# Optimization experiments

Hardware: AMD Instinct MI355X
Metric: run time of the kernel (lower is better)

Reference implementation:

```python
import jax, jax.numpy as jnp
import numpy as np

D = 1352      # d_model
H = 8         # n_heads
HD = D // H   # 169 head dim
L = 7         # n_layers
E = 4         # experts per layer
DFF = 2704    # expert hidden (2*d_model)
NUM_OPS = 16
OP_START = 0
B, S = 1, 1024


def setup_inputs() -> dict:
    key = jax.random.key(0)
    ks = jax.random.split(key, 8)
    g = lambda k, shape, sc: (jax.random.normal(k, shape, jnp.float32) * sc)
    return {
        "x": g(ks[0], (B, S, D), 1.0),
        "ln1_g": jnp.ones((L, D), jnp.float32),
        "ln1_b": jnp.zeros((L, D), jnp.float32),
        "wqkv": g(ks[1], (L, D, 3 * D), 0.02),
        "bqkv": jnp.zeros((L, 3 * D), jnp.float32),
        "wo": g(ks[2], (L, D, D), 0.02),
        "bo": jnp.zeros((L, D), jnp.float32),
        "ln2_g": jnp.ones((L, D), jnp.float32),
        "ln2_b": jnp.zeros((L, D), jnp.float32),
        "w1": g(ks[3], (L, E, D, DFF), 0.02),
        "b1": jnp.zeros((L, E, DFF), jnp.float32),
        "w2": g(ks[4], (L, E, DFF, D), 0.02),
        "b2": jnp.zeros((L, E, D), jnp.float32),
    }


def _layer_norm(x, g, b, eps=1e-5):
    mu = jnp.mean(x, axis=-1, keepdims=True)
    var = jnp.mean(jnp.square(x - mu), axis=-1, keepdims=True)
    return (x - mu) * jax.lax.rsqrt(var + eps) * g + b


def reference(x, ln1_g, ln1_b, wqkv, bqkv, wo, bo, ln2_g, ln2_b, w1, b1, w2, b2):
    Bx, Sx, _ = x.shape
    # deterministic opcode routing: one-hot slab -> opcode id -> expert id
    op_ids = jnp.argmax(x[..., OP_START:OP_START + NUM_OPS], axis=-1)  # [B,S]
    mask = jax.nn.one_hot(op_ids % E, E, dtype=x.dtype)                # [B,S,E]
    causal = jnp.tril(jnp.ones((Sx, Sx), bool))
    neg = jnp.asarray(-1e9, x.dtype)
    scale = jnp.asarray(1.0 / np.sqrt(HD), x.dtype)

    def block(h, p):
        g1, bb1, wq, bq, w_o, b_o, g2, bb2, W1, B1, W2, B2 = p
        # --- causal multi-head attention (pre-LN, residual) ---
        a = _layer_norm(h, g1, bb1)
        qkv = a @ wq + bq                                   # [B,S,3D]
        q, k, v = jnp.split(qkv, 3, axis=-1)
        q = q.reshape(Bx, Sx, H, HD).transpose(0, 2, 1, 3)  # [B,H,S,HD]
        k = k.reshape(Bx, Sx, H, HD).transpose(0, 2, 1, 3)
        v = v.reshape(Bx, Sx, H, HD).transpose(0, 2, 1, 3)
        scores = jnp.einsum("bhqd,bhkd->bhqk", q, k) * scale
        scores = jnp.where(causal, scores, neg)
        attn = jax.nn.softmax(scores, axis=-1)
        o = jnp.einsum("bhqk,bhkd->bhqd", attn, v)
        o = o.transpose(0, 2, 1, 3).reshape(Bx, Sx, D) @ w_o + b_o
        h = h + o
        # --- opcode-routed MoE FFN (dense masked compute, one-hot dispatch) ---
        m = _layer_norm(h, g2, bb2)
        hid = jax.nn.relu(jnp.einsum("bsd,edf->bsef", m, W1) + B1)   # [B,S,E,DFF]
        y = jnp.einsum("bsef,efd->bsed", hid, W2) + B2               # [B,S,E,D]
        h = h + jnp.einsum("bsed,bse->bsd", y, mask)
        return h, None

    out, _ = jax.lax.scan(
        block, x,
        (ln1_g, ln1_b, wqkv, bqkv, wo, bo, ln2_g, ln2_b, w1, b1, w2, b2),
    )
    return out
```

## Files before the change

### kernel.cpp

```cpp
#include <hip/hip_runtime.h>
#include <hip/hip_bf16.h>
#include <cstdint>

#define S_LEN 1024
#define DMODEL 1352
#define TD 4056
#define DFFN 2704
#define NHEAD 8
#define HDIM 169
#define NLAYER 7
#define LDAP 1408
#define KP2 2752
#define QS 1536
#define HP 192

typedef __attribute__((ext_vector_type(8))) short short8;
typedef __attribute__((ext_vector_type(4))) float f32x4;
typedef __attribute__((ext_vector_type(2))) unsigned short us2;
typedef __attribute__((ext_vector_type(4))) unsigned short us4;

__device__ __forceinline__ unsigned short f2bf(float f) {
    union { float f; unsigned int u; } c; c.f = f;
    unsigned int r = (c.u + 0x7fffu + ((c.u >> 16) & 1u)) >> 16;
    return (unsigned short)r;
}

__device__ __forceinline__ float bf2f(unsigned short u) {
    union { unsigned int u; float f; } c; c.u = (unsigned int)u << 16;
    return c.f;
}

__device__ __forceinline__ void g2l16(const void* g, void* l) {
    __builtin_amdgcn_global_load_lds((__attribute__((address_space(1))) void*)g,
                                     (__attribute__((address_space(3))) void*)l,
                                     16, 0, 0);
}

__global__ __launch_bounds__(256) void route_k(const float* __restrict__ x,
                                               int* __restrict__ perm,
                                               int* __restrict__ pcnt) {
    const int tid = threadIdx.x;
    const int lane = tid & 63;
    const int w = tid >> 6;
    for (int i = tid; i < 4096; i += 256) perm[i] = -1;
    __syncthreads();
    int base = 0;
    for (int c = 0; c < 16; ++c) {
        const int t = c * 64 + lane;
        const float* xr = x + (long long)t * DMODEL;
        float best = xr[0]; int bi = 0;
        #pragma unroll
        for (int j = 1; j < 16; ++j) { float v = xr[j]; if (v > best) { best = v; bi = j; } }
        const bool match = ((bi & 3) == w);
        unsigned long long mb = __ballot(match);
        int pos = __popcll(mb & ((1ull << lane) - 1ull));
        if (match) perm[w * 1024 + base + pos] = t;
        base += __popcll(mb);
    }
    if (lane == 0) pcnt[w] = (base + 127) & ~127;
}

__device__ __forceinline__ void tconv_tile64(const float* __restrict__ src,
    unsigned short* __restrict__ dst, int K, int N, int Kp, int kt, int nt,
    float (*t)[65])
{
    const int k0 = kt * 32, n0 = nt * 64;
    const int lane = threadIdx.x & 63, wv = threadIdx.x >> 6;
    #pragma unroll
    for (int i = 0; i < 8; ++i) {
        const int k = k0 + wv * 8 + i;
        const int n = n0 + lane;
        t[wv * 8 + i][lane] = (k < K && n < N) ? src[(long long)k * N + n] : 0.f;
    }
    __syncthreads();
    #pragma unroll
    for (int p = 0; p < 4; ++p) {
        const int nr = p * 16 + (threadIdx.x >> 4);
        const int kp = (threadIdx.x & 15) * 2;
        const int n = n0 + nr;
        if (n < N) {
            us2 wv2; wv2.x = f2bf(t[kp][nr]); wv2.y = f2bf(t[kp + 1][nr]);
            *(us2*)&dst[(long long)n * Kp + k0 + kp] = wv2;
        }
    }
}

__device__ __forceinline__ void ln_row(const float* __restrict__ h,
    const float* __restrict__ g, const float* __restrict__ b,
    unsigned short* __restrict__ out, int row, float* sA, float* sB)
{
    const float* hr = h + (long long)row * DMODEL;
    float s = 0.f, s2 = 0.f;
    for (int j = threadIdx.x; j < DMODEL; j += 256) { float v = hr[j]; s += v; s2 += v * v; }
    #pragma unroll
    for (int o = 32; o; o >>= 1) { s += __shfl_xor(s, o, 64); s2 += __shfl_xor(s2, o, 64); }
    const int lane = threadIdx.x & 63, wid = threadIdx.x >> 6;
    if (lane == 0) { sA[wid] = s; sB[wid] = s2; }
    __syncthreads();
    s = sA[0] + sA[1] + sA[2] + sA[3];
    s2 = sB[0] + sB[1] + sB[2] + sB[3];
    const float mu = s / DMODEL;
    const float rstd = rsqrtf(fmaxf(s2 / DMODEL - mu * mu, 0.f) + 1e-5f);
    unsigned short* orow = out + (long long)row * LDAP;
    for (int j = threadIdx.x; j < LDAP; j += 256) {
        float v = (j < DMODEL) ? (hr[j] - mu) * rstd * g[j] + b[j] : 0.f;
        orow[j] = f2bf(v);
    }
}

#define NB1_QKV (44 * 64)
#define NB1_WO  (44 * 22)
#define NB2_W1  (44 * 43 * 4)
#define NB2_W2  (86 * 22 * 4)

__global__ __launch_bounds__(256) void prep1_k(
    const float* __restrict__ wqkv_l, const float* __restrict__ wo_l,
    unsigned short* __restrict__ wqkvT, unsigned short* __restrict__ woT,
    const float* __restrict__ h, const float* __restrict__ g,
    const float* __restrict__ bb, unsigned short* __restrict__ lnA)
{
    __shared__ __align__(16) float t[32][65];
    __shared__ float sA[4], sB[4];
    int b = blockIdx.x;
    if (b < NB1_QKV) {
        tconv_tile64(wqkv_l, wqkvT, DMODEL, TD, LDAP, b % 44, b / 44, t);
        return;
    }
    b -= NB1_QKV;
    if (b < NB1_WO) {
        tconv_tile64(wo_l, woT, DMODEL, DMODEL, LDAP, b % 44, b / 44, t);
        return;
    }
    b -= NB1_WO;
    ln_row(h, g, bb, lnA, b, sA, sB);
}

__global__ __launch_bounds__(256) void prep2_k(
    const float* __restrict__ w1_l, const float* __restrict__ w2_l,
    unsigned short* __restrict__ w1T, unsigned short* __restrict__ w2T,
    const float* __restrict__ h, const float* __restrict__ g,
    const float* __restrict__ bb, unsigned short* __restrict__ lnA)
{
    __shared__ __align__(16) float t[32][65];
    __shared__ float sA[4], sB[4];
    int b = blockIdx.x;
    if (b < NB2_W1) {
        const int kt = b % 44, rem = b / 44;
        const int nt = rem % 43, z = rem / 43;
        tconv_tile64(w1_l + (long long)z * DMODEL * DFFN,
                     w1T + (long long)z * 2816 * LDAP,
                     DMODEL, DFFN, LDAP, kt, nt, t);
        return;
    }
    b -= NB2_W1;
    if (b < NB2_W2) {
        const int kt = b % 86, rem = b / 86;
        const int nt = rem % 22, z = rem / 22;
        tconv_tile64(w2_l + (long long)z * DFFN * DMODEL,
                     w2T + (long long)z * 1408 * KP2,
                     DFFN, DMODEL, KP2, kt, nt, t);
        return;
    }
    b -= NB2_W2;
    ln_row(h, g, bb, lnA, b, sA, sB);
}

__global__ __launch_bounds__(256) void softmax_k(const unsigned short* __restrict__ scores,
                                                 unsigned short* __restrict__ P,
                                                 float scale) {
    const int i = blockIdx.x;
    const long long rb = ((long long)blockIdx.y * 1024 + i) * 1024;
    const unsigned short* srow = scores + rb;
    unsigned short* prow = P + rb;
    const int n = i + 1;
    const int j0 = threadIdx.x * 4;

    us4 raw = *(const us4*)&srow[j0];
    float v[4];
    #pragma unroll
    for (int e = 0; e < 4; ++e)
        v[e] = (j0 + e < n) ? bf2f(raw[e]) * scale : -1e30f;

    float mx = fmaxf(fmaxf(v[0], v[1]), fmaxf(v[2], v[3]));
    __shared__ float sA[4], sB[4];
    #pragma unroll
    for (int o = 32; o; o >>= 1) mx = fmaxf(mx, __shfl_xor(mx, o, 64));
    const int lane = threadIdx.x & 63, wid = threadIdx.x >> 6;
    if (lane == 0) sA[wid] = mx;
    __syncthreads();
    mx = fmaxf(fmaxf(sA[0], sA[1]), fmaxf(sA[2], sA[3]));

    float p[4]; float sum = 0.f;
    #pragma unroll
    for (int e = 0; e < 4; ++e) {
        p[e] = (j0 + e < n) ? __expf(v[e] - mx) : 0.f;
        sum += p[e];
    }
    #pragma unroll
    for (int o = 32; o; o >>= 1) sum += __shfl_xor(sum, o, 64);
    if (lane == 0) sB[wid] = sum;
    __syncthreads();
    const float inv = 1.f / (sB[0] + sB[1] + sB[2] + sB[3]);

    us4 out;
    #pragma unroll
    for (int e = 0; e < 4; ++e) out[e] = f2bf(p[e] * inv);
    *(us4*)&prow[j0] = out;
}

template<int EPI, bool GATHER, int CAUSAL>
__global__ __launch_bounds__(512) void gemm2_k(
    const unsigned short* __restrict__ A_, int lda, long long zsA,
    const unsigned short* __restrict__ B_, int ldb, long long zsB,
    void* __restrict__ C_, int ldc, long long zsC,
    const float* __restrict__ bias_, long long zsBias,
    const int* __restrict__ perm_, const int* __restrict__ pcnt,
    int N, int Kp,
    unsigned short* __restrict__ q_, unsigned short* __restrict__ k_,
    unsigned short* __restrict__ vt_) {
    const int z = blockIdx.z;
    const int gm0 = blockIdx.y * 64;
    const int n0 = blockIdx.x * 128;
    if (pcnt && gm0 >= pcnt[z]) return;
    if (CAUSAL == 1 && n0 >= gm0 + 64) return;

    const unsigned short* A = A_ + (long long)z * zsA;
    const unsigned short* B = B_ + (long long)z * zsB;
    const float* bias = bias_ ? bias_ + (long long)z * zsBias : nullptr;
    const int* perm = perm_ ? perm_ + (long long)z * 1024 : nullptr;

    __shared__ unsigned short Al[2][64 * 64];
    __shared__ unsigned short Bl[2][128 * 64];

    const int tid = threadIdx.x, lane = tid & 63, wid = tid >> 6;
    const int wr = wid >> 2, wc = wid & 3;
    const int l15 = lane & 15, lg = lane >> 4;

    const int sr = lane >> 3;
    const int scs = (lane & 7) ^ sr;

    const unsigned short* gA;
    {
        const int row = wid * 8 + sr;
        int ar = gm0 + row;
        if (GATHER) { const int p = perm[ar]; ar = (p < 0) ? 0 : p; }
        gA = A + (long long)ar * lda + scs * 8;
    }
    const unsigned short* gB[2];
    #pragma unroll
    for (int j = 0; j < 2; ++j)
        gB[j] = B + (long long)(n0 + wid * 16 + j * 8 + sr) * ldb + scs * 8;

    const int ldsA = wid * 512;
    const int ldsB = wid * 1024;

    int nt = Kp >> 6;
    if (CAUSAL == 2) { int ke = gm0 + 64; if (ke > Kp) ke = Kp; nt = ke >> 6; }

    f32x4 acc[2][2] = {};

    #pragma unroll
    for (int tt = 0; tt < 2; ++tt) {
        const int ts = (tt < nt) ? tt : nt - 1;
        const int ko = ts * 64;
        g2l16(gA + ko, &Al[tt & 1][ldsA]);
        g2l16(gB[0] + ko, &Bl[tt & 1][ldsB]);
        g2l16(gB[1] + ko, &Bl[tt & 1][ldsB + 512]);
    }

    for (int t = 0; t < nt; ++t) {
        asm volatile("s_waitcnt vmcnt(3)" ::: "memory");
        __builtin_amdgcn_s_barrier();
        __builtin_amdgcn_sched_barrier(0);
        const int cur = t & 1;
        short8 af[2][2], bfv[2][2];
        #pragma unroll
        for (int m = 0; m < 2; ++m)
            #pragma unroll
            for (int s = 0; s < 2; ++s)
                af[m][s] = *(const short8*)&Al[cur][(wr * 32 + m * 16 + l15) * 64 +
                                                    (((s * 4 + lg) ^ (l15 & 7)) * 8)];
        #pragma unroll
        for (int n = 0; n < 2; ++n)
            #pragma unroll
            for (int s = 0; s < 2; ++s)
                bfv[n][s] = *(const short8*)&Bl[cur][(wc * 32 + n * 16 + l15) * 64 +
                                                     (((s * 4 + lg) ^ (l15 & 7)) * 8)];
        #pragma unroll
        for (int s = 0; s < 2; ++s)
            #pragma unroll
            for (int m = 0; m < 2; ++m)
                #pragma unroll
                for (int n = 0; n < 2; ++n)
                    acc[m][n] = __builtin_amdgcn_mfma_f32_16x16x32_bf16(af[m][s], bfv[n][s], acc[m][n], 0, 0, 0);
        __builtin_amdgcn_sched_barrier(0);
        __builtin_amdgcn_s_barrier();
        __builtin_amdgcn_sched_barrier(0);
        {
            const int ts = (t + 2 < nt) ? t + 2 : nt - 1;
            const int ko = ts * 64;
            g2l16(gA + ko, &Al[cur][ldsA]);
            g2l16(gB[0] + ko, &Bl[cur][ldsB]);
            g2l16(gB[1] + ko, &Bl[cur][ldsB + 512]);
        }
    }

    asm volatile("s_waitcnt vmcnt(0) lgkmcnt(0)" ::: "memory");

    const int lq = lg * 4;
    #pragma unroll
    for (int m = 0; m < 2; ++m) {
        const int trow = wr * 32 + m * 16 + lq;
        #pragma unroll
        for (int n = 0; n < 2; ++n) {
            const int col = n0 + wc * 32 + n * 16 + l15;
            if (col >= N) continue;
            const float bv = bias ? bias[col] : 0.f;
            if (EPI == 5) {
                const int role = col / 1352;
                const int within = col - role * 1352;
                const int hh = within / 169;
                const int dd = within - hh * 169;
                if (role == 2) {
                    us4 pk;
                    #pragma unroll
                    for (int r = 0; r < 4; ++r) pk[r] = f2bf(acc[m][n][r] + bv);
                    *(us4*)&vt_[(long long)(hh * 256 + dd) * 1024 + gm0 + trow] = pk;
                } else {
                    unsigned short* dstb = role ? k_ : q_;
                    #pragma unroll
                    for (int r = 0; r < 4; ++r)
                        dstb[(long long)(gm0 + trow + r) * QS + hh * HP + dd] =
                            f2bf(acc[m][n][r] + bv);
                }
            } else {
                #pragma unroll
                for (int r = 0; r < 4; ++r) {
                    const int grow = gm0 + trow + r;
                    const float v = acc[m][n][r] + bv;
                    if (EPI == 0) {
                        ((float*)C_)[(long long)z * zsC + (long long)grow * ldc + col] = v;
                    } else if (EPI == 1) {
                        const int tok = perm[grow];
                        ((unsigned short*)C_)[(long long)z * zsC + (long long)grow * ldc + col] =
                            (tok >= 0) ? f2bf(fmaxf(v, 0.f)) : (unsigned short)0;
                    } else if (EPI == 2) {
                        ((float*)C_)[(long long)grow * ldc + col] += v;
                    } else if (EPI == 3) {
                        const int tok = perm[grow];
                        if (tok >= 0) ((float*)C_)[(long long)tok * ldc + col] += v;
                    } else if (EPI == 6) {
                        ((unsigned short*)C_)[(long long)grow * ldc + z * 169 + col] = f2bf(v);
                    } else if (EPI == 7) {
                        ((unsigned short*)C_)[(long long)z * zsC + (long long)grow * ldc + col] = f2bf(v);
                    }
                }
            }
        }
    }
}

extern "C" void kernel_launch(void* const* d_in, const int* in_sizes, int n_in,
                              void* d_out, int out_size, void* d_ws, size_t ws_size,
                              hipStream_t stream) {
    const float* x     = (const float*)d_in[0];
    const float* ln1_g = (const float*)d_in[1];
    const float* ln1_b = (const float*)d_in[2];
    const float* wqkv  = (const float*)d_in[3];
    const float* bqkv  = (const float*)d_in[4];
    const float* wo    = (const float*)d_in[5];
    const float* bo    = (const float*)d_in[6];
    const float* ln2_g = (const float*)d_in[7];
    const float* ln2_b = (const float*)d_in[8];
    const float* w1    = (const float*)d_in[9];
    const float* b1    = (const float*)d_in[10];
    const float* w2    = (const float*)d_in[11];
    const float* b2    = (const float*)d_in[12];

    float* h = (float*)d_out;

    char* w = (char*)d_ws;
    auto alloc = [&](size_t bytes) { void* p = w; w += (bytes + 255) & ~255ull; return p; };
    unsigned short* lnA   = (unsigned short*)alloc((size_t)S_LEN * LDAP * 2);
    unsigned short* qb    = (unsigned short*)alloc((size_t)S_LEN * QS * 2);
    unsigned short* kb    = (unsigned short*)alloc((size_t)S_LEN * QS * 2);
    unsigned short* VT    = (unsigned short*)alloc((size_t)NHEAD * 256 * 1024 * 2);
    unsigned short* obufb = (unsigned short*)alloc((size_t)S_LEN * LDAP * 2);
    unsigned short* hid   = (unsigned short*)alloc((size_t)4096 * KP2 * 2);
    unsigned short* wqkvT = (unsigned short*)alloc((size_t)4096 * LDAP * 2);
    unsigned short* woT   = (unsigned short*)alloc((size_t)1408 * LDAP * 2);
    char*           U     = (char*)alloc((size_t)64000000);
    int* perm = (int*)alloc(4096 * 4);
    int* pcnt = (int*)alloc(64);

    unsigned short* scoresb = (unsigned short*)U;
    unsigned short* Pbuf    = (unsigned short*)(U + (size_t)NHEAD * 1024 * 1024 * 2);
    unsigned short* w1T     = (unsigned short*)U;
    unsigned short* w2T     = (unsigned short*)(U + (size_t)4 * 2816 * LDAP * 2);

    hipMemcpyAsync(h, x, (size_t)S_LEN * DMODEL * 4, hipMemcpyDeviceToDevice, stream);
    hipMemsetAsync(qb, 0, (size_t)S_LEN * QS * 2, stream);
    hipMemsetAsync(kb, 0, (size_t)S_LEN * QS * 2, stream);
    route_k<<<1, 256, 0, stream>>>(x, perm, pcnt);

    const float scale = 1.0f / 13.0f;

    for (int l = 0; l < NLAYER; ++l) {
        const float* wqkv_l = wqkv + (long long)l * DMODEL * TD;
        const float* wo_l   = wo   + (long long)l * DMODEL * DMODEL;
        const float* w1_l   = w1   + (long long)l * 4 * DMODEL * DFFN;
        const float* w2_l   = w2   + (long long)l * 4 * DFFN * DMODEL;

        prep1_k<<<NB1_QKV + NB1_WO + 1024, 256, 0, stream>>>(
            wqkv_l, wo_l, wqkvT, woT, h, ln1_g + l * DMODEL, ln1_b + l * DMODEL, lnA);
        gemm2_k<5, false, 0><<<dim3(32, 16, 1), 512, 0, stream>>>(
            lnA, LDAP, 0, wqkvT, LDAP, 0, nullptr, 0, 0,
            bqkv + l * TD, 0, nullptr, nullptr, TD, LDAP, qb, kb, VT);
        gemm2_k<7, false, 1><<<dim3(8, 16, 8), 512, 0, stream>>>(
            qb, QS, HP, kb, QS, HP, scoresb, 1024, 1024 * 1024,
            nullptr, 0, nullptr, nullptr, 1024, HP, nullptr, nullptr, nullptr);
        softmax_k<<<dim3(1024, NHEAD), 256, 0, stream>>>(scoresb, Pbuf, scale);
        gemm2_k<6, false, 2><<<dim3(2, 16, 8), 512, 0, stream>>>(
            Pbuf, 1024, 1024 * 1024, VT, 1024, 256 * 1024, obufb, LDAP, 0,
            nullptr, 0, nullptr, nullptr, HDIM, 1024, nullptr, nullptr, nullptr);
        gemm2_k<2, false, 0><<<dim3(11, 16, 1), 512, 0, stream>>>(
            obufb, LDAP, 0, woT, LDAP, 0, h, DMODEL, 0,
            bo + l * DMODEL, 0, nullptr, nullptr, DMODEL, LDAP, nullptr, nullptr, nullptr);

        prep2_k<<<NB2_W1 + NB2_W2 + 1024, 256, 0, stream>>>(
            w1_l, w2_l, w1T, w2T, h, ln2_g + l * DMODEL, ln2_b + l * DMODEL, lnA);
        gemm2_k<1, true, 0><<<dim3(22, 16, 4), 512, 0, stream>>>(
            lnA, LDAP, 0, w1T, LDAP, (long long)2816 * LDAP,
            hid, KP2, (long long)1024 * KP2,
            b1 + (long long)l * 4 * DFFN, DFFN, perm, pcnt, DFFN, LDAP,
            nullptr, nullptr, nullptr);
        gemm2_k<3, false, 0><<<dim3(11, 16, 4), 512, 0, stream>>>(
            hid, KP2, (long long)1024 * KP2, w2T, KP2, (long long)1408 * KP2,
            h, DMODEL, 0,
            b2 + (long long)l * 4 * DMODEL, DMODEL, perm, pcnt, DMODEL, KP2,
            nullptr, nullptr, nullptr);
    }
}
```

Measured before the change: 1.606 ms.

## Fuse causal softmax into the P·V kernel per 64-row query block

```diff
diff --git a/kernel.cpp b/kernel.cpp
--- a/kernel.cpp
+++ b/kernel.cpp
@@ -165,47 +165,153 @@
     ln_row(h, g, bb, lnA, b, sA, sB);
 }
 
-__global__ __launch_bounds__(256) void softmax_k(const unsigned short* __restrict__ scores,
-                                                 unsigned short* __restrict__ P,
-                                                 float scale) {
-    const int i = blockIdx.x;
-    const long long rb = ((long long)blockIdx.y * 1024 + i) * 1024;
-    const unsigned short* srow = scores + rb;
-    unsigned short* prow = P + rb;
-    const int n = i + 1;
-    const int j0 = threadIdx.x * 4;
-
-    us4 raw = *(const us4*)&srow[j0];
-    float v[4];
-    #pragma unroll
-    for (int e = 0; e < 4; ++e)
-        v[e] = (j0 + e < n) ? bf2f(raw[e]) * scale : -1e30f;
-
-    float mx = fmaxf(fmaxf(v[0], v[1]), fmaxf(v[2], v[3]));
-    __shared__ float sA[4], sB[4];
-    #pragma unroll
-    for (int o = 32; o; o >>= 1) mx = fmaxf(mx, __shfl_xor(mx, o, 64));
-    const int lane = threadIdx.x & 63, wid = threadIdx.x >> 6;
-    if (lane == 0) sA[wid] = mx;
-    __syncthreads();
-    mx = fmaxf(fmaxf(sA[0], sA[1]), fmaxf(sA[2], sA[3]));
-
-    float p[4]; float sum = 0.f;
-    #pragma unroll
-    for (int e = 0; e < 4; ++e) {
-        p[e] = (j0 + e < n) ? __expf(v[e] - mx) : 0.f;
-        sum += p[e];
-    }
-    #pragma unroll
-    for (int o = 32; o; o >>= 1) sum += __shfl_xor(sum, o, 64);
-    if (lane == 0) sB[wid] = sum;
-    __syncthreads();
-    const float inv = 1.f / (sB[0] + sB[1] + sB[2] + sB[3]);
-
-    us4 out;
-    #pragma unroll
-    for (int e = 0; e < 4; ++e) out[e] = f2bf(p[e] * inv);
-    *(us4*)&prow[j0] = out;
+__global__ __launch_bounds__(512) void pv_k(
+    const unsigned short* __restrict__ scoresb,
+    const unsigned short* __restrict__ Pbuf_,
+    unsigned short* __restrict__ Pw,
+    const unsigned short* __restrict__ VT,
+    unsigned short* __restrict__ obuf,
+    float scale)
+{
+    const int z = blockIdx.y;
+    const int gm0 = blockIdx.x * 64;
+    const int kEnd = gm0 + 64;
+    const int tid = threadIdx.x, lane = tid & 63, wid = tid >> 6;
+    const int wr = wid >> 2, wc = wid & 3;
+    const int l15 = lane & 15, lg = lane >> 4;
+
+    const unsigned short* Sb = scoresb + (long long)z * 1024 * 1024;
+    unsigned short* Pb = Pw + (long long)z * 1024 * 1024;
+
+    const float sc = scale;
+    for (int i = 0; i < 8; ++i) {
+        const int q = gm0 + wid * 8 + i;
+        const int n = q + 1;
+        const unsigned short* srow = Sb + (long long)q * 1024;
+        unsigned short* prow = Pb + (long long)q * 1024;
+        float v[16];
+        float mx = -1e30f;
+        for (int s = 0; s < 4; ++s) {
+            const int col = s * 256 + lane * 4;
+            if (col < kEnd) {
+                us4 raw = *(const us4*)&srow[col];
+                #pragma unroll
+                for (int e = 0; e < 4; ++e) {
+                    float x = (col + e < n) ? bf2f(raw[e]) * sc : -1e30f;
+                    v[s * 4 + e] = x;
+                    mx = fmaxf(mx, x);
+                }
+            } else {
+                #pragma unroll
+                for (int e = 0; e < 4; ++e) v[s * 4 + e] = -1e30f;
+            }
+        }
+        #pragma unroll
+        for (int o = 32; o; o >>= 1) mx = fmaxf(mx, __shfl_xor(mx, o, 64));
+        float sum = 0.f;
+        #pragma unroll
+        for (int j = 0; j < 16; ++j) {
+            float p = (v[j] > -1e29f) ? __expf(v[j] - mx) : 0.f;
+            v[j] = p; sum += p;
+        }
+        #pragma unroll
+        for (int o = 32; o; o >>= 1) sum += __shfl_xor(sum, o, 64);
+        const float inv = 1.f / sum;
+        for (int s = 0; s < 4; ++s) {
+            const int col = s * 256 + lane * 4;
+            if (col < kEnd) {
+                us4 out;
+                #pragma unroll
+                for (int e = 0; e < 4; ++e) out[e] = f2bf(v[s * 4 + e] * inv);
+                *(us4*)&prow[col] = out;
+            }
+        }
+    }
+    asm volatile("s_waitcnt vmcnt(0)" ::: "memory");
+
+    __shared__ unsigned short Al[2][64 * 64];
+    __shared__ unsigned short Bl[2][192 * 64];
+
+    const int sr = lane >> 3;
+    const int scs = (lane & 7) ^ sr;
+
+    const unsigned short* gA = Pb + (long long)(gm0 + wid * 8 + sr) * 1024 + scs * 8;
+    const unsigned short* gB[3];
+    #pragma unroll
+    for (int j = 0; j < 3; ++j)
+        gB[j] = VT + (long long)(z * 256 + wid * 24 + j * 8 + sr) * 1024 + scs * 8;
+
+    const int ldsA = wid * 512;
+    const int ldsB = wid * 1536;
+
+    const int nt = kEnd >> 6;
+    f32x4 acc[2][3] = {};
+
+    #pragma unroll
+    for (int tt = 0; tt < 2; ++tt) {
+        const int ts = (tt < nt) ? tt : nt - 1;
+        const int ko = ts * 64;
+        g2l16(gA + ko, &Al[tt & 1][ldsA]);
+        #pragma unroll
+        for (int j = 0; j < 3; ++j)
+            g2l16(gB[j] + ko, &Bl[tt & 1][ldsB + j * 512]);
+    }
+
+    for (int t = 0; t < nt; ++t) {
+        asm volatile("s_waitcnt vmcnt(4)" ::: "memory");
+        __builtin_amdgcn_s_barrier();
+        __builtin_amdgcn_sched_barrier(0);
+        const int cur = t & 1;
+        short8 af[2][2], bfv[3][2];
+        #pragma unroll
+        for (int m = 0; m < 2; ++m)
+            #pragma unroll
+            for (int s = 0; s < 2; ++s)
+                af[m][s] = *(const short8*)&Al[cur][(wr * 32 + m * 16 + l15) * 64 +
+                                                    (((s * 4 + lg) ^ (l15 & 7)) * 8)];
+        #pragma unroll
+        for (int n = 0; n < 3; ++n)
+            #pragma unroll
+            for (int s = 0; s < 2; ++s)
+                bfv[n][s] = *(const short8*)&Bl[cur][(wc * 48 + n * 16 + l15) * 64 +
+                                                     (((s * 4 + lg) ^ (l15 & 7)) * 8)];
+        #pragma unroll
+        for (int s = 0; s < 2; ++s)
+            #pragma unroll
+            for (int m = 0; m < 2; ++m)
+                #pragma unroll
+                for (int n = 0; n < 3; ++n)
+                    acc[m][n] = __builtin_amdgcn_mfma_f32_16x16x32_bf16(af[m][s], bfv[n][s], acc[m][n], 0, 0, 0);
+        __builtin_amdgcn_sched_barrier(0);
+        __builtin_amdgcn_s_barrier();
+        __builtin_amdgcn_sched_barrier(0);
+        {
+            const int ts = (t + 2 < nt) ? t + 2 : nt - 1;
+            const int ko = ts * 64;
+            g2l16(gA + ko, &Al[cur][ldsA]);
+            #pragma unroll
+            for (int j = 0; j < 3; ++j)
+                g2l16(gB[j] + ko, &Bl[cur][ldsB + j * 512]);
+        }
+    }
+
+    asm volatile("s_waitcnt vmcnt(0) lgkmcnt(0)" ::: "memory");
+
+    const int lq = lg * 4;
+    #pragma unroll
+    for (int m = 0; m < 2; ++m) {
+        const int trow = wr * 32 + m * 16 + lq;
+        #pragma unroll
+        for (int n = 0; n < 3; ++n) {
+            const int col = wc * 48 + n * 16 + l15;
+            if (col >= HDIM) continue;
+            #pragma unroll
+            for (int r = 0; r < 4; ++r) {
+                const int q = gm0 + trow + r;
+                obuf[(long long)q * LDAP + z * HDIM + col] = f2bf(acc[m][n][r]);
+            }
+        }
+    }
 }
 
 template<int EPI, bool GATHER, int CAUSAL>
@@ -349,8 +455,6 @@
                     } else if (EPI == 3) {
                         const int tok = perm[grow];
                         if (tok >= 0) ((float*)C_)[(long long)tok * ldc + col] += v;
-                    } else if (EPI == 6) {
-                        ((unsigned short*)C_)[(long long)grow * ldc + z * 169 + col] = f2bf(v);
                     } else if (EPI == 7) {
                         ((unsigned short*)C_)[(long long)z * zsC + (long long)grow * ldc + col] = f2bf(v);
                     }
@@ -419,10 +523,7 @@
         gemm2_k<7, false, 1><<<dim3(8, 16, 8), 512, 0, stream>>>(
             qb, QS, HP, kb, QS, HP, scoresb, 1024, 1024 * 1024,
             nullptr, 0, nullptr, nullptr, 1024, HP, nullptr, nullptr, nullptr);
-        softmax_k<<<dim3(1024, NHEAD), 256, 0, stream>>>(scoresb, Pbuf, scale);
-        gemm2_k<6, false, 2><<<dim3(2, 16, 8), 512, 0, stream>>>(
-            Pbuf, 1024, 1024 * 1024, VT, 1024, 256 * 1024, obufb, LDAP, 0,
-            nullptr, 0, nullptr, nullptr, HDIM, 1024, nullptr, nullptr, nullptr);
+        pv_k<<<dim3(16, NHEAD), 512, 0, stream>>>(scoresb, Pbuf, Pbuf, VT, obufb, scale);
         gemm2_k<2, false, 0><<<dim3(11, 16, 1), 512, 0, stream>>>(
             obufb, LDAP, 0, woT, LDAP, 0, h, DMODEL, 0,
             bo + l * DMODEL, 0, nullptr, nullptr, DMODEL, LDAP, nullptr, nullptr, nullptr);
```

Result: slower. 1.658 ms (+3.2%).
